# Optimization experiments

Hardware: AMD Instinct MI355X
Metric: run time of the kernel (lower is better)

The kernel has to match this reference:

```python
import jax, jax.numpy as jnp
import numpy as np

B, L, H_IN, H_RED, H_MLP = 2, 1024, 768, 128, 256

def setup_inputs() -> dict:
    key = jax.random.key(0)
    ks = jax.random.split(key, 7)
    s_in = 1.0 / np.sqrt(H_IN)
    s_p = 1.0 / np.sqrt(2 * H_RED)
    s_m = 1.0 / np.sqrt(H_MLP)
    return {
        "inputs": jax.random.normal(ks[0], (B, L, H_IN), dtype=jnp.float32),
        "Wr": jax.random.uniform(ks[1], (H_RED, H_IN), jnp.float32, -s_in, s_in),
        "br": jax.random.uniform(ks[2], (H_RED,), jnp.float32, -s_in, s_in),
        "W1": jax.random.uniform(ks[3], (H_MLP, 2 * H_RED), jnp.float32, -s_p, s_p),
        "b1": jax.random.uniform(ks[4], (H_MLP,), jnp.float32, -s_p, s_p),
        "W2": jax.random.uniform(ks[5], (1, H_MLP), jnp.float32, -s_m, s_m),
        "b2": jax.random.uniform(ks[6], (1,), jnp.float32, -s_m, s_m),
    }

def reference(inputs, Wr, br, W1, b1, W2, b2):
    # pre_reduction: [B,L,H_IN] -> [B,L,H_RED]
    e = jnp.einsum("blh,rh->blr", inputs, Wr) + br
    b_, l_, r_ = e.shape
    # pairwise concat: row i gets e[i], col j gets e[j] -> [B,L,L,2R]
    row = jnp.broadcast_to(e[:, :, None, :], (b_, l_, l_, r_))
    col = jnp.broadcast_to(e[:, None, :, :], (b_, l_, l_, r_))
    pair = jnp.concatenate([row, col], axis=-1)
    # Lin2D: Linear(2R,256) -> ReLU -> Linear(256,1)
    h = jax.nn.relu(jnp.einsum("bijc,mc->bijm", pair, W1) + b1)
    out = jnp.einsum("bijm,om->bijo", h, W2) + b2  # [B,L,L,1]
    out = out[..., 0]  # [B,L,L]
    # symmetrize: triu(out) + triu(out,1)^T
    upper = jnp.triu(out)
    lower = jnp.swapaxes(jnp.triu(out, k=1), -1, -2)
    return upper + lower
```

## Files before the change

kernel.cpp:

```cpp
#include <hip/hip_runtime.h>

typedef __attribute__((ext_vector_type(4))) float f32x4;
typedef __attribute__((ext_vector_type(8))) short bf16x8;

__device__ inline unsigned short f2bf(float x) {
  unsigned u = __builtin_bit_cast(unsigned, x);
  u += 0x7fffu + ((u >> 16) & 1u);
  return (unsigned short)(u >> 16);
}

__device__ inline bf16x8 pack8(f32x4 lo, f32x4 hi) {
  bf16x8 r;
  r[0] = (short)f2bf(lo[0]); r[1] = (short)f2bf(lo[1]);
  r[2] = (short)f2bf(lo[2]); r[3] = (short)f2bf(lo[3]);
  r[4] = (short)f2bf(hi[0]); r[5] = (short)f2bf(hi[1]);
  r[6] = (short)f2bf(hi[2]); r[7] = (short)f2bf(hi[3]);
  return r;
}

__global__ __launch_bounds__(256) void prep_kernel(
    const float* __restrict__ X, const float* __restrict__ Wr,
    const float* __restrict__ W1, const float* __restrict__ W2,
    unsigned short* __restrict__ Xbf, unsigned short* __restrict__ Wrbf,
    unsigned short* __restrict__ W1bf, float* __restrict__ w2h) {
  int bid = blockIdx.x, tid = threadIdx.x;
  if (bid < 768) {
    size_t o = (size_t)bid * 2048 + tid * 8;
    f32x4 a = *(const f32x4*)(X + o), b = *(const f32x4*)(X + o + 4);
    *(bf16x8*)(Xbf + o) = pack8(a, b);
  } else if (bid < 816) {
    size_t o = (size_t)(bid - 768) * 2048 + tid * 8;
    f32x4 a = *(const f32x4*)(Wr + o), b = *(const f32x4*)(Wr + o + 4);
    *(bf16x8*)(Wrbf + o) = pack8(a, b);
  } else if (bid < 848) {
    size_t o = (size_t)(bid - 816) * 2048 + tid * 8;
    int m = (int)(o >> 7), k = (int)(o & 127);
    const float* src = (m < 256) ? (W1 + (size_t)m * 256 + k)
                                 : (W1 + (size_t)(m - 256) * 256 + 128 + k);
    f32x4 a = *(const f32x4*)src, b = *(const f32x4*)(src + 4);
    *(bf16x8*)(W1bf + o) = pack8(a, b);
  } else {
    w2h[tid] = 0.5f * W2[tid];
  }
}

__global__ __launch_bounds__(256) void gemm1_kernel(
    const unsigned short* __restrict__ Xbf, const unsigned short* __restrict__ Wrbf,
    const float* __restrict__ br, unsigned short* __restrict__ Ebf) {
  int wave = threadIdx.x >> 6, lane = threadIdx.x & 63;
  int tok0 = (blockIdx.x * 4 + wave) * 16;
  int n0 = blockIdx.y * 64;
  int lr = lane & 15, kg = (lane >> 4) * 8;
  const unsigned short* ap = Xbf + (size_t)(tok0 + lr) * 768 + kg;
  const unsigned short* bp0 = Wrbf + (size_t)(n0 + lr) * 768 + kg;
  const unsigned short* bp1 = bp0 + 16 * 768;
  const unsigned short* bp2 = bp0 + 32 * 768;
  const unsigned short* bp3 = bp0 + 48 * 768;
  f32x4 acc0 = {0,0,0,0}, acc1 = {0,0,0,0}, acc2 = {0,0,0,0}, acc3 = {0,0,0,0};
#pragma unroll 4
  for (int k0 = 0; k0 < 768; k0 += 32) {
    bf16x8 a = *(const bf16x8*)(ap + k0);
    bf16x8 b0 = *(const bf16x8*)(bp0 + k0);
    bf16x8 b1 = *(const bf16x8*)(bp1 + k0);
    bf16x8 b2 = *(const bf16x8*)(bp2 + k0);
    bf16x8 b3 = *(const bf16x8*)(bp3 + k0);
    acc0 = __builtin_amdgcn_mfma_f32_16x16x32_bf16(a, b0, acc0, 0, 0, 0);
    acc1 = __builtin_amdgcn_mfma_f32_16x16x32_bf16(a, b1, acc1, 0, 0, 0);
    acc2 = __builtin_amdgcn_mfma_f32_16x16x32_bf16(a, b2, acc2, 0, 0, 0);
    acc3 = __builtin_amdgcn_mfma_f32_16x16x32_bf16(a, b3, acc3, 0, 0, 0);
  }
  int rb = (lane >> 4) * 4;
  f32x4 accs[4] = {acc0, acc1, acc2, acc3};
#pragma unroll
  for (int t = 0; t < 4; ++t) {
    int n = n0 + t * 16 + lr;
    float bias = br[n];
#pragma unroll
    for (int r = 0; r < 4; ++r)
      Ebf[(size_t)(tok0 + rb + r) * 128 + n] = f2bf(accs[t][r] + bias);
  }
}

__global__ __launch_bounds__(256) void gemm2_kernel(
    const unsigned short* __restrict__ Ebf, const unsigned short* __restrict__ W1bf,
    const float* __restrict__ b1, const float* __restrict__ w2h,
    float* __restrict__ UVt, float* __restrict__ cvec) {
  int wave = threadIdx.x >> 6, lane = threadIdx.x & 63;
  int t0 = blockIdx.x * 64;
  int m0 = (blockIdx.y * 4 + wave) * 16;
  int lr = lane & 15, kg = (lane >> 4) * 8;
  const unsigned short* aB = W1bf + (size_t)(m0 + lr) * 128 + kg;
  f32x4 acc[4] = {{0,0,0,0},{0,0,0,0},{0,0,0,0},{0,0,0,0}};
#pragma unroll
  for (int k0 = 0; k0 < 128; k0 += 32) {
    bf16x8 a = *(const bf16x8*)(aB + k0);
#pragma unroll
    for (int t = 0; t < 4; ++t) {
      bf16x8 b = *(const bf16x8*)(Ebf + (size_t)(t0 + t * 16 + lr) * 128 + kg + k0);
      acc[t] = __builtin_amdgcn_mfma_f32_16x16x32_bf16(a, b, acc[t], 0, 0, 0);
    }
  }
  int rb = (lane >> 4) * 4;
  float p[4] = {0.f, 0.f, 0.f, 0.f};
#pragma unroll
  for (int t = 0; t < 4; ++t) {
#pragma unroll
    for (int r = 0; r < 4; ++r) {
      int m = m0 + rb + r;
      float val = acc[t][r] + ((m0 < 256) ? b1[m] : 0.f);
      UVt[(size_t)m * 2048 + t0 + t * 16 + lr] = val;
      p[t] = fmaf(w2h[m & 255], val, p[t]);
    }
  }
#pragma unroll
  for (int t = 0; t < 4; ++t) {
    p[t] += __shfl_xor(p[t], 16);
    p[t] += __shfl_xor(p[t], 32);
  }
  if (lane < 16) {
    int h = (m0 < 256) ? 0 : 1;
#pragma unroll
    for (int t = 0; t < 4; ++t)
      atomicAdd(&cvec[h * 2048 + t0 + t * 16 + lane], p[t]);
  }
}

__global__ __launch_bounds__(256) void pairwise_kernel(
    const float* __restrict__ UVt, const float* __restrict__ w2h,
    const float* __restrict__ cvec, const float* __restrict__ b2p,
    float* __restrict__ Out) {
  __shared__ float u_s[4][64][36];
  __shared__ float v_s[4][64][36];
  __shared__ float w2_s[256];
  __shared__ float cuv[64];

  int tid = threadIdx.x;
  int wave = tid >> 6, lane = tid & 63;
  int b = blockIdx.y;
  int p = blockIdx.x;
  int it = 0;
  while (p >= 32 - it) { p -= 32 - it; ++it; }
  int jt = it + p;

  int utok = b * 1024 + it * 32;
  int vtok = b * 1024 + jt * 32;

  w2_s[tid] = w2h[tid];
  if (tid < 32) cuv[tid] = cvec[utok + tid];
  else if (tid < 64) cuv[tid] = cvec[2048 + vtok + (tid - 32)];

  int mr = lane >> 3, tq = (lane & 7) * 4;
#pragma unroll
  for (int g = 0; g < 8; ++g) {
    int ml = g * 8 + mr;
    int m = wave * 64 + ml;
    *(f32x4*)&u_s[wave][ml][tq] = *(const f32x4*)(UVt + (size_t)m * 2048 + utok + tq);
    *(f32x4*)&v_s[wave][ml][tq] = *(const f32x4*)(UVt + (size_t)(256 + m) * 2048 + vtok + tq);
  }
  __syncthreads();

  int tx = lane & 7, ty = lane >> 3;
  float acc[4][4] = {{0,0,0,0},{0,0,0,0},{0,0,0,0},{0,0,0,0}};
  for (int ml = 0; ml < 64; ml += 4) {
    f32x4 wq = *(const f32x4*)&w2_s[wave * 64 + ml];
#pragma unroll
    for (int s = 0; s < 4; ++s) {
      f32x4 uu = *(const f32x4*)&u_s[wave][ml + s][4 * ty];
      f32x4 vv = *(const f32x4*)&v_s[wave][ml + s][4 * tx];
      float w = wq[s];
#pragma unroll
      for (int i = 0; i < 4; ++i)
#pragma unroll
        for (int j = 0; j < 4; ++j)
          acc[i][j] = fmaf(w, fabsf(uu[i] + vv[j]), acc[i][j]);
    }
  }

  __syncthreads();
  float* ov = (float*)u_s;
  if (wave > 0) {
#pragma unroll
    for (int i = 0; i < 4; ++i) {
      f32x4 rowv = {acc[i][0], acc[i][1], acc[i][2], acc[i][3]};
      *(f32x4*)&ov[(((wave - 1) * 4 + i) * 64 + lane) * 4] = rowv;
    }
  }
  __syncthreads();
  if (wave == 0) {
#pragma unroll
    for (int w = 1; w < 4; ++w)
#pragma unroll
      for (int i = 0; i < 4; ++i) {
        f32x4 rowv = *(const f32x4*)&ov[(((w - 1) * 4 + i) * 64 + lane) * 4];
#pragma unroll
        for (int j = 0; j < 4; ++j) acc[i][j] += rowv[j];
      }
    float b2v = b2p[0];
    float val[4][4];
#pragma unroll
    for (int i = 0; i < 4; ++i)
#pragma unroll
      for (int j = 0; j < 4; ++j)
        val[i][j] = acc[i][j] + cuv[4 * ty + i] + cuv[32 + 4 * tx + j] + b2v;

    size_t obase = (size_t)b << 20;
    int i0 = it * 32, j0 = jt * 32;
    if (it != jt) {
#pragma unroll
      for (int i = 0; i < 4; ++i) {
        f32x4 dv = {val[i][0], val[i][1], val[i][2], val[i][3]};
        *(f32x4*)(Out + obase + (size_t)(i0 + 4 * ty + i) * 1024 + j0 + 4 * tx) = dv;
      }
      float* t32 = (float*)v_s;
#pragma unroll
      for (int i = 0; i < 4; ++i)
#pragma unroll
        for (int j = 0; j < 4; ++j)
          t32[(4 * ty + i) * 33 + 4 * tx + j] = val[i][j];
      __builtin_amdgcn_s_waitcnt(0);
#pragma unroll
      for (int i = 0; i < 4; ++i) {
        f32x4 mv;
#pragma unroll
        for (int k = 0; k < 4; ++k) mv[k] = t32[(4 * tx + k) * 33 + 4 * ty + i];
        *(f32x4*)(Out + obase + (size_t)(j0 + 4 * ty + i) * 1024 + i0 + 4 * tx) = mv;
      }
    } else {
#pragma unroll
      for (int i = 0; i < 4; ++i)
#pragma unroll
        for (int j = 0; j < 4; ++j) {
          int il = 4 * ty + i, jl = 4 * tx + j;
          if (jl >= il) Out[obase + (size_t)(i0 + il) * 1024 + j0 + jl] = val[i][j];
          if (jl > il)  Out[obase + (size_t)(j0 + jl) * 1024 + i0 + il] = val[i][j];
        }
    }
  }
}

extern "C" void kernel_launch(void* const* d_in, const int* in_sizes, int n_in,
                              void* d_out, int out_size, void* d_ws, size_t ws_size,
                              hipStream_t stream) {
  (void)in_sizes; (void)n_in; (void)out_size; (void)ws_size;
  const float* X  = (const float*)d_in[0];
  const float* Wr = (const float*)d_in[1];
  const float* br = (const float*)d_in[2];
  const float* W1 = (const float*)d_in[3];
  const float* b1 = (const float*)d_in[4];
  const float* W2 = (const float*)d_in[5];
  const float* b2 = (const float*)d_in[6];
  float* Out = (float*)d_out;

  char* ws = (char*)d_ws;
  unsigned short* Xbf  = (unsigned short*)(ws);
  unsigned short* Wrbf = (unsigned short*)(ws + 3145728);
  unsigned short* W1bf = (unsigned short*)(ws + 3342336);
  float*          w2h  = (float*)(ws + 3473408);
  unsigned short* Ebf  = (unsigned short*)(ws + 3474432);
  float*          UVt  = (float*)(ws + 3998720);
  float*          cvec = (float*)(ws + 8193024);

  prep_kernel<<<849, 256, 0, stream>>>(X, Wr, W1, W2, Xbf, Wrbf, W1bf, w2h);
  hipMemsetAsync(cvec, 0, 2 * 2048 * sizeof(float), stream);
  gemm1_kernel<<<dim3(32, 2), 256, 0, stream>>>(Xbf, Wrbf, br, Ebf);
  gemm2_kernel<<<dim3(32, 8), 256, 0, stream>>>(Ebf, W1bf, b1, w2h, UVt, cvec);
  pairwise_kernel<<<dim3(528, 2), 256, 0, stream>>>(UVt, w2h, cvec, b2, Out);
}
```

Baseline: 64.99 us.

## Fuse prep, both GEMMs and c-vector reduction into one kernel; parallelize pairwise epilogue

New measurement: 74.15 us. +14.1%, slower.

```diff
diff --git a/kernel.cpp b/kernel.cpp
--- a/kernel.cpp
+++ b/kernel.cpp
@@ -18,115 +18,112 @@
   return r;
 }
 
-__global__ __launch_bounds__(256) void prep_kernel(
+__device__ inline bf16x8 cvt8(const float* __restrict__ p) {
+  return pack8(*(const f32x4*)p, *(const f32x4*)(p + 4));
+}
+
+__global__ __launch_bounds__(256) void fused_gemm_kernel(
     const float* __restrict__ X, const float* __restrict__ Wr,
-    const float* __restrict__ W1, const float* __restrict__ W2,
-    unsigned short* __restrict__ Xbf, unsigned short* __restrict__ Wrbf,
-    unsigned short* __restrict__ W1bf, float* __restrict__ w2h) {
-  int bid = blockIdx.x, tid = threadIdx.x;
-  if (bid < 768) {
-    size_t o = (size_t)bid * 2048 + tid * 8;
-    f32x4 a = *(const f32x4*)(X + o), b = *(const f32x4*)(X + o + 4);
-    *(bf16x8*)(Xbf + o) = pack8(a, b);
-  } else if (bid < 816) {
-    size_t o = (size_t)(bid - 768) * 2048 + tid * 8;
-    f32x4 a = *(const f32x4*)(Wr + o), b = *(const f32x4*)(Wr + o + 4);
-    *(bf16x8*)(Wrbf + o) = pack8(a, b);
-  } else if (bid < 848) {
-    size_t o = (size_t)(bid - 816) * 2048 + tid * 8;
-    int m = (int)(o >> 7), k = (int)(o & 127);
-    const float* src = (m < 256) ? (W1 + (size_t)m * 256 + k)
-                                 : (W1 + (size_t)(m - 256) * 256 + 128 + k);
-    f32x4 a = *(const f32x4*)src, b = *(const f32x4*)(src + 4);
-    *(bf16x8*)(W1bf + o) = pack8(a, b);
-  } else {
-    w2h[tid] = 0.5f * W2[tid];
-  }
-}
-
-__global__ __launch_bounds__(256) void gemm1_kernel(
-    const unsigned short* __restrict__ Xbf, const unsigned short* __restrict__ Wrbf,
-    const float* __restrict__ br, unsigned short* __restrict__ Ebf) {
-  int wave = threadIdx.x >> 6, lane = threadIdx.x & 63;
-  int tok0 = (blockIdx.x * 4 + wave) * 16;
-  int n0 = blockIdx.y * 64;
+    const float* __restrict__ br, const float* __restrict__ W1,
+    const float* __restrict__ b1, const float* __restrict__ W2,
+    float* __restrict__ UVt, float* __restrict__ cvec) {
+  __shared__ unsigned short Ws[128][264];
+  __shared__ unsigned short e_s[32][136];
+  __shared__ float cvp[4][32];
+
+  int tid = threadIdx.x, wave = tid >> 6, lane = tid & 63;
+  int T0 = blockIdx.x * 32;
   int lr = lane & 15, kg = (lane >> 4) * 8;
-  const unsigned short* ap = Xbf + (size_t)(tok0 + lr) * 768 + kg;
-  const unsigned short* bp0 = Wrbf + (size_t)(n0 + lr) * 768 + kg;
-  const unsigned short* bp1 = bp0 + 16 * 768;
-  const unsigned short* bp2 = bp0 + 32 * 768;
-  const unsigned short* bp3 = bp0 + 48 * 768;
+  int strip = wave >> 1, nh = wave & 1;
+
+  const float* xrow = X + (size_t)(T0 + strip * 16 + lr) * 768 + kg;
   f32x4 acc0 = {0,0,0,0}, acc1 = {0,0,0,0}, acc2 = {0,0,0,0}, acc3 = {0,0,0,0};
-#pragma unroll 4
-  for (int k0 = 0; k0 < 768; k0 += 32) {
-    bf16x8 a = *(const bf16x8*)(ap + k0);
-    bf16x8 b0 = *(const bf16x8*)(bp0 + k0);
-    bf16x8 b1 = *(const bf16x8*)(bp1 + k0);
-    bf16x8 b2 = *(const bf16x8*)(bp2 + k0);
-    bf16x8 b3 = *(const bf16x8*)(bp3 + k0);
-    acc0 = __builtin_amdgcn_mfma_f32_16x16x32_bf16(a, b0, acc0, 0, 0, 0);
-    acc1 = __builtin_amdgcn_mfma_f32_16x16x32_bf16(a, b1, acc1, 0, 0, 0);
-    acc2 = __builtin_amdgcn_mfma_f32_16x16x32_bf16(a, b2, acc2, 0, 0, 0);
-    acc3 = __builtin_amdgcn_mfma_f32_16x16x32_bf16(a, b3, acc3, 0, 0, 0);
-  }
+
+  for (int c = 0; c < 3; ++c) {
+    __syncthreads();
+#pragma unroll
+    for (int i = 0; i < 16; ++i) {
+      int base = (tid + 256 * i) * 8;
+      int row = base >> 8, col = base & 255;
+      const float* src = Wr + (size_t)row * 768 + c * 256 + col;
+      *(bf16x8*)&Ws[row][col] = pack8(*(const f32x4*)src, *(const f32x4*)(src + 4));
+    }
+    __syncthreads();
+#pragma unroll
+    for (int s = 0; s < 8; ++s) {
+      bf16x8 a = cvt8(xrow + c * 256 + s * 32);
+      bf16x8 b0 = *(const bf16x8*)&Ws[nh * 64 + lr][s * 32 + kg];
+      bf16x8 b1f = *(const bf16x8*)&Ws[nh * 64 + 16 + lr][s * 32 + kg];
+      bf16x8 b2f = *(const bf16x8*)&Ws[nh * 64 + 32 + lr][s * 32 + kg];
+      bf16x8 b3f = *(const bf16x8*)&Ws[nh * 64 + 48 + lr][s * 32 + kg];
+      acc0 = __builtin_amdgcn_mfma_f32_16x16x32_bf16(a, b0, acc0, 0, 0, 0);
+      acc1 = __builtin_amdgcn_mfma_f32_16x16x32_bf16(a, b1f, acc1, 0, 0, 0);
+      acc2 = __builtin_amdgcn_mfma_f32_16x16x32_bf16(a, b2f, acc2, 0, 0, 0);
+      acc3 = __builtin_amdgcn_mfma_f32_16x16x32_bf16(a, b3f, acc3, 0, 0, 0);
+    }
+  }
+
   int rb = (lane >> 4) * 4;
-  f32x4 accs[4] = {acc0, acc1, acc2, acc3};
-#pragma unroll
-  for (int t = 0; t < 4; ++t) {
-    int n = n0 + t * 16 + lr;
-    float bias = br[n];
-#pragma unroll
-    for (int r = 0; r < 4; ++r)
-      Ebf[(size_t)(tok0 + rb + r) * 128 + n] = f2bf(accs[t][r] + bias);
-  }
-}
-
-__global__ __launch_bounds__(256) void gemm2_kernel(
-    const unsigned short* __restrict__ Ebf, const unsigned short* __restrict__ W1bf,
-    const float* __restrict__ b1, const float* __restrict__ w2h,
-    float* __restrict__ UVt, float* __restrict__ cvec) {
-  int wave = threadIdx.x >> 6, lane = threadIdx.x & 63;
-  int t0 = blockIdx.x * 64;
-  int m0 = (blockIdx.y * 4 + wave) * 16;
-  int lr = lane & 15, kg = (lane >> 4) * 8;
-  const unsigned short* aB = W1bf + (size_t)(m0 + lr) * 128 + kg;
-  f32x4 acc[4] = {{0,0,0,0},{0,0,0,0},{0,0,0,0},{0,0,0,0}};
-#pragma unroll
-  for (int k0 = 0; k0 < 128; k0 += 32) {
-    bf16x8 a = *(const bf16x8*)(aB + k0);
+  {
+    f32x4 accs[4] = {acc0, acc1, acc2, acc3};
 #pragma unroll
     for (int t = 0; t < 4; ++t) {
-      bf16x8 b = *(const bf16x8*)(Ebf + (size_t)(t0 + t * 16 + lr) * 128 + kg + k0);
-      acc[t] = __builtin_amdgcn_mfma_f32_16x16x32_bf16(a, b, acc[t], 0, 0, 0);
-    }
-  }
-  int rb = (lane >> 4) * 4;
-  float p[4] = {0.f, 0.f, 0.f, 0.f};
-#pragma unroll
-  for (int t = 0; t < 4; ++t) {
+      int n = nh * 64 + t * 16 + lr;
+      float bias = br[n];
+#pragma unroll
+      for (int r = 0; r < 4; ++r)
+        e_s[strip * 16 + rb + r][n] = f2bf(accs[t][r] + bias);
+    }
+  }
+  __syncthreads();
+
+  bf16x8 bfr[2][4];
+#pragma unroll
+  for (int tt = 0; tt < 2; ++tt)
+#pragma unroll
+    for (int kk = 0; kk < 4; ++kk)
+      bfr[tt][kk] = *(const bf16x8*)&e_s[tt * 16 + lr][kk * 32 + kg];
+
+  int M0 = wave * 128;
+  float p0 = 0.f, p1 = 0.f;
+#pragma unroll
+  for (int mt = 0; mt < 8; ++mt) {
+    int m1 = M0 + mt * 16;
+    const float* arow = (m1 < 256)
+        ? W1 + (size_t)(m1 + lr) * 256 + kg
+        : W1 + (size_t)(m1 - 256 + lr) * 256 + 128 + kg;
+    f32x4 ac0 = {0,0,0,0}, ac1 = {0,0,0,0};
+#pragma unroll
+    for (int kk = 0; kk < 4; ++kk) {
+      bf16x8 a = cvt8(arow + kk * 32);
+      ac0 = __builtin_amdgcn_mfma_f32_16x16x32_bf16(a, bfr[0][kk], ac0, 0, 0, 0);
+      ac1 = __builtin_amdgcn_mfma_f32_16x16x32_bf16(a, bfr[1][kk], ac1, 0, 0, 0);
+    }
 #pragma unroll
     for (int r = 0; r < 4; ++r) {
-      int m = m0 + rb + r;
-      float val = acc[t][r] + ((m0 < 256) ? b1[m] : 0.f);
-      UVt[(size_t)m * 2048 + t0 + t * 16 + lr] = val;
-      p[t] = fmaf(w2h[m & 255], val, p[t]);
-    }
-  }
-#pragma unroll
-  for (int t = 0; t < 4; ++t) {
-    p[t] += __shfl_xor(p[t], 16);
-    p[t] += __shfl_xor(p[t], 32);
-  }
-  if (lane < 16) {
-    int h = (m0 < 256) ? 0 : 1;
-#pragma unroll
-    for (int t = 0; t < 4; ++t)
-      atomicAdd(&cvec[h * 2048 + t0 + t * 16 + lane], p[t]);
-  }
-}
-
-__global__ __launch_bounds__(256) void pairwise_kernel(
-    const float* __restrict__ UVt, const float* __restrict__ w2h,
+      int m = m1 + rb + r;
+      float bias = (m < 256) ? b1[m] : 0.f;
+      float w2v = W2[m & 255];
+      float v0 = ac0[r] + bias;
+      float v1 = ac1[r] + bias;
+      UVt[(size_t)m * 2048 + T0 + lr] = v0;
+      UVt[(size_t)m * 2048 + T0 + 16 + lr] = v1;
+      p0 = fmaf(w2v, v0, p0);
+      p1 = fmaf(w2v, v1, p1);
+    }
+  }
+  p0 += __shfl_xor(p0, 16); p0 += __shfl_xor(p0, 32);
+  p1 += __shfl_xor(p1, 16); p1 += __shfl_xor(p1, 32);
+  if (lane < 16) { cvp[wave][lr] = p0; cvp[wave][16 + lr] = p1; }
+  __syncthreads();
+  if (tid < 64) {
+    int h = tid >> 5, tok = tid & 31;
+    cvec[h * 2048 + T0 + tok] = 0.5f * (cvp[2 * h][tok] + cvp[2 * h + 1][tok]);
+  }
+}
+
+__global__ __launch_bounds__(256, 2) void pairwise_kernel(
+    const float* __restrict__ UVt, const float* __restrict__ W2,
     const float* __restrict__ cvec, const float* __restrict__ b2p,
     float* __restrict__ Out) {
   __shared__ float u_s[4][64][36];
@@ -145,11 +142,15 @@
   int utok = b * 1024 + it * 32;
   int vtok = b * 1024 + jt * 32;
 
-  w2_s[tid] = w2h[tid];
+  w2_s[tid] = W2[tid];
   if (tid < 32) cuv[tid] = cvec[utok + tid];
   else if (tid < 64) cuv[tid] = cvec[2048 + vtok + (tid - 32)];
+  __syncthreads();
 
   int mr = lane >> 3, tq = (lane & 7) * 4;
+  int tx = lane & 7, ty = lane >> 3;
+  float acc[4][4] = {{0,0,0,0},{0,0,0,0},{0,0,0,0},{0,0,0,0}};
+
 #pragma unroll
   for (int g = 0; g < 8; ++g) {
     int ml = g * 8 + mr;
@@ -157,10 +158,7 @@
     *(f32x4*)&u_s[wave][ml][tq] = *(const f32x4*)(UVt + (size_t)m * 2048 + utok + tq);
     *(f32x4*)&v_s[wave][ml][tq] = *(const f32x4*)(UVt + (size_t)(256 + m) * 2048 + vtok + tq);
   }
-  __syncthreads();
-
-  int tx = lane & 7, ty = lane >> 3;
-  float acc[4][4] = {{0,0,0,0},{0,0,0,0},{0,0,0,0},{0,0,0,0}};
+
   for (int ml = 0; ml < 64; ml += 4) {
     f32x4 wq = *(const f32x4*)&w2_s[wave * 64 + ml];
 #pragma unroll
@@ -176,64 +174,56 @@
     }
   }
 
-  __syncthreads();
-  float* ov = (float*)u_s;
-  if (wave > 0) {
-#pragma unroll
-    for (int i = 0; i < 4; ++i) {
-      f32x4 rowv = {acc[i][0], acc[i][1], acc[i][2], acc[i][3]};
-      *(f32x4*)&ov[(((wave - 1) * 4 + i) * 64 + lane) * 4] = rowv;
-    }
-  }
-  __syncthreads();
-  if (wave == 0) {
-#pragma unroll
-    for (int w = 1; w < 4; ++w)
-#pragma unroll
-      for (int i = 0; i < 4; ++i) {
-        f32x4 rowv = *(const f32x4*)&ov[(((w - 1) * 4 + i) * 64 + lane) * 4];
-#pragma unroll
-        for (int j = 0; j < 4; ++j) acc[i][j] += rowv[j];
-      }
-    float b2v = b2p[0];
-    float val[4][4];
-#pragma unroll
-    for (int i = 0; i < 4; ++i)
-#pragma unroll
-      for (int j = 0; j < 4; ++j)
-        val[i][j] = acc[i][j] + cuv[4 * ty + i] + cuv[32 + 4 * tx + j] + b2v;
-
-    size_t obase = (size_t)b << 20;
-    int i0 = it * 32, j0 = jt * 32;
-    if (it != jt) {
-#pragma unroll
-      for (int i = 0; i < 4; ++i) {
-        f32x4 dv = {val[i][0], val[i][1], val[i][2], val[i][3]};
-        *(f32x4*)(Out + obase + (size_t)(i0 + 4 * ty + i) * 1024 + j0 + 4 * tx) = dv;
-      }
-      float* t32 = (float*)v_s;
-#pragma unroll
-      for (int i = 0; i < 4; ++i)
-#pragma unroll
-        for (int j = 0; j < 4; ++j)
-          t32[(4 * ty + i) * 33 + 4 * tx + j] = val[i][j];
-      __builtin_amdgcn_s_waitcnt(0);
-#pragma unroll
-      for (int i = 0; i < 4; ++i) {
-        f32x4 mv;
-#pragma unroll
-        for (int k = 0; k < 4; ++k) mv[k] = t32[(4 * tx + k) * 33 + 4 * ty + i];
-        *(f32x4*)(Out + obase + (size_t)(j0 + 4 * ty + i) * 1024 + i0 + 4 * tx) = mv;
-      }
-    } else {
-#pragma unroll
-      for (int i = 0; i < 4; ++i)
-#pragma unroll
-        for (int j = 0; j < 4; ++j) {
-          int il = 4 * ty + i, jl = 4 * tx + j;
-          if (jl >= il) Out[obase + (size_t)(i0 + il) * 1024 + j0 + jl] = val[i][j];
-          if (jl > il)  Out[obase + (size_t)(j0 + jl) * 1024 + i0 + il] = val[i][j];
-        }
+  float* ovp = (float*)u_s;
+  float* t2p = (float*)v_s;
+  __syncthreads();
+#pragma unroll
+  for (int i = 0; i < 4; ++i) {
+    f32x4 rv = {acc[i][0], acc[i][1], acc[i][2], acc[i][3]};
+    *(f32x4*)&ovp[((size_t)wave * 32 + 4 * ty + i) * 36 + 4 * tx] = rv;
+  }
+  __syncthreads();
+
+  int ly = lane >> 3, tc = lane & 7;
+  int row = wave * 8 + ly;
+  float b2v = b2p[0];
+  f32x4 sum = {0,0,0,0};
+#pragma unroll
+  for (int q = 0; q < 4; ++q) {
+    f32x4 part = *(const f32x4*)&ovp[((size_t)q * 32 + row) * 36 + 4 * tc];
+#pragma unroll
+    for (int j = 0; j < 4; ++j) sum[j] += part[j];
+  }
+  float cu = cuv[row];
+  f32x4 val;
+#pragma unroll
+  for (int j = 0; j < 4; ++j)
+    val[j] = 0.5f * sum[j] + cu + cuv[32 + 4 * tc + j] + b2v;
+
+  *(f32x4*)&t2p[(size_t)row * 36 + 4 * tc] = val;
+
+  size_t obase = (size_t)b << 20;
+  int i0 = it * 32, j0 = jt * 32;
+  if (it != jt)
+    *(f32x4*)(Out + obase + (size_t)(i0 + row) * 1024 + j0 + 4 * tc) = val;
+  else {
+#pragma unroll
+    for (int j = 0; j < 4; ++j) {
+      int jl = 4 * tc + j;
+      if (jl >= row) Out[obase + (size_t)(i0 + row) * 1024 + j0 + jl] = val[j];
+    }
+  }
+  __syncthreads();
+  f32x4 mv;
+#pragma unroll
+  for (int j = 0; j < 4; ++j) mv[j] = t2p[(size_t)(4 * tc + j) * 36 + row];
+  if (it != jt)
+    *(f32x4*)(Out + obase + (size_t)(j0 + row) * 1024 + i0 + 4 * tc) = mv;
+  else {
+#pragma unroll
+    for (int j = 0; j < 4; ++j) {
+      int c = 4 * tc + j;
+      if (row > c) Out[obase + (size_t)(i0 + row) * 1024 + j0 + c] = mv[j];
     }
   }
 }
@@ -251,18 +241,9 @@
   const float* b2 = (const float*)d_in[6];
   float* Out = (float*)d_out;
 
-  char* ws = (char*)d_ws;
-  unsigned short* Xbf  = (unsigned short*)(ws);
-  unsigned short* Wrbf = (unsigned short*)(ws + 3145728);
-  unsigned short* W1bf = (unsigned short*)(ws + 3342336);
-  float*          w2h  = (float*)(ws + 3473408);
-  unsigned short* Ebf  = (unsigned short*)(ws + 3474432);
-  float*          UVt  = (float*)(ws + 3998720);
-  float*          cvec = (float*)(ws + 8193024);
-
-  prep_kernel<<<849, 256, 0, stream>>>(X, Wr, W1, W2, Xbf, Wrbf, W1bf, w2h);
-  hipMemsetAsync(cvec, 0, 2 * 2048 * sizeof(float), stream);
-  gemm1_kernel<<<dim3(32, 2), 256, 0, stream>>>(Xbf, Wrbf, br, Ebf);
-  gemm2_kernel<<<dim3(32, 8), 256, 0, stream>>>(Ebf, W1bf, b1, w2h, UVt, cvec);
-  pairwise_kernel<<<dim3(528, 2), 256, 0, stream>>>(UVt, w2h, cvec, b2, Out);
-}
+  float* UVt  = (float*)d_ws;
+  float* cvec = (float*)((char*)d_ws + (size_t)512 * 2048 * 4);
+
+  fused_gemm_kernel<<<64, 256, 0, stream>>>(X, Wr, br, W1, b1, W2, UVt, cvec);
+  pairwise_kernel<<<dim3(528, 2), 256, 0, stream>>>(UVt, W2, cvec, b2, Out);
+}
```
